# Kernel optimization log

Hardware: AMD Instinct MI355X
Metric: run time of the kernel (lower is better)

## Reference

```python
import jax, jax.numpy as jnp
import numpy as np

L = 32          # ss_num: number of sampled layers
D = 512         # lstm_size
OPS = 16        # operations_num
TEMP = 5.0
TANH_C = 2.5
OP_TANH_RED = 2.5
NEG = jnp.float32(-1e9)  # finite mask value (avoids inf/nan in grads)


def setup_inputs() -> dict:
    key = jax.random.key(0)
    ks = jax.random.split(key, 9)
    u = lambda k, s: jax.random.uniform(k, s, jnp.float32, -0.1, 0.1)  # reset_param: uniform(-0.1, 0.1)
    return {
        "embedding": u(ks[0], (OPS + 1, D)),
        "w_ih": u(ks[1], (4 * D, D)),
        "w_hh": u(ks[2], (4 * D, D)),
        "b_ih": u(ks[3], (4 * D,)),
        "b_hh": u(ks[4], (4 * D,)),
        "w_attn_1": u(ks[5], (D, D)),
        "w_attn_2": u(ks[6], (D, D)),
        "index_fc": u(ks[7], (D,)),
        "op_fc": u(ks[8], (OPS, D)),
    }


def _lstm_cell(x, h, c, w_ih, w_hh, b_ih, b_hh):
    # torch.nn.LSTMCell: gate order i, f, g, o
    g = x @ w_ih.T + b_ih + h @ w_hh.T + b_hh
    i, f, gg, o = jnp.split(g, 4, axis=-1)
    c2 = jax.nn.sigmoid(f) * c + jax.nn.sigmoid(i) * jnp.tanh(gg)
    h2 = jax.nn.sigmoid(o) * jnp.tanh(c2)
    return h2, c2


def reference(embedding, w_ih, w_hh, b_ih, b_hh, w_attn_1, w_attn_2, index_fc, op_fc):
    cell = lambda x, h, c: _lstm_cell(x, h, c, w_ih, w_hh, b_ih, b_hh)
    skey = jax.random.key(42)

    # --- initial construct_node (prev state = zeros) ---
    inp0 = embedding[OPS]                 # embedding of sentinel token [D]
    h, c = cell(inp0, jnp.zeros((D,), jnp.float32), jnp.zeros((D,), jnp.float32))
    anchors = jnp.zeros((L + 1, D), jnp.float32)            # anchor[0] = zeros_like(h)
    anchors_w1 = jnp.zeros((L + 1, D), jnp.float32).at[0].set(h @ w_attn_1.T)

    def step(carry, t):
        h, c, inp, anchors, anchors_w1, key = carry
        k1, k2, key = jax.random.split(key, 3)
        valid = jnp.arange(L + 1) <= t  # anchors 0..t exist at layer t

        # node selection
        h, c = cell(inp, h, c)
        query = jnp.tanh(anchors_w1 + h @ w_attn_2.T)        # [L+1, D]
        idx_logits = (query @ index_fc) / TEMP               # [L+1]
        idx_logits = TANH_C * jnp.tanh(idx_logits)
        idx_logits = jnp.where(valid, idx_logits, NEG)
        node_idx = jax.random.categorical(k1, idx_logits)
        lsm = jax.nn.log_softmax(idx_logits)
        node_lp = -lsm[node_idx]                             # cross_entropy
        node_ent = -jnp.sum(jnp.where(valid, lsm, 0.0) * jnp.exp(lsm))

        # op selection
        op_in = anchors[node_idx]
        h, c = cell(op_in, h, c)
        op_logits = (h @ op_fc.T) / TEMP
        op_logits = (TANH_C / OP_TANH_RED) * jnp.tanh(op_logits)
        op_idx = jax.random.categorical(k2, op_logits)
        olsm = jax.nn.log_softmax(op_logits)
        op_lp = -olsm[op_idx]
        op_ent = -jnp.sum(olsm * jnp.exp(olsm))

        inp = embedding[op_idx]
        anchors = anchors.at[t + 1].set(h)
        anchors_w1 = anchors_w1.at[t + 1].set(h @ w_attn_1.T)
        ent = jax.lax.stop_gradient(node_ent + op_ent)       # entropy is .detach()ed
        return (h, c, inp, anchors, anchors_w1, key), (node_idx, op_idx, node_lp + op_lp, ent)

    carry0 = (h, c, inp0, anchors, anchors_w1, skey)
    _, (nidx, oidx, lps, ents) = jax.lax.scan(step, carry0, jnp.arange(L))
    arch_seq = jnp.stack([nidx, oidx], axis=1).reshape(-1)   # interleave [node, op] x L
    return arch_seq, jnp.sum(ents), jnp.sum(lps)
```

## Files before the change

kernel.cpp:

```cpp
#include <hip/hip_runtime.h>
#include <stdint.h>


#define KWG    64
#define NTH    512
#define LSTEPS 32
#define DDIM   512
#define NOPS   16
#define NEGC   (-1.0e9f)

static __device__ __forceinline__ void tf2x32(uint32_t k0, uint32_t k1,
                                              uint32_t c0, uint32_t c1,
                                              uint32_t& o0, uint32_t& o1){
  uint32_t ks2 = k0 ^ k1 ^ 0x1BD11BDAu;
  uint32_t x0 = c0 + k0;
  uint32_t x1 = c1 + k1;
#define TFR(r) { x0 += x1; x1 = (x1 << (r)) | (x1 >> (32 - (r))); x1 ^= x0; }
  TFR(13) TFR(15) TFR(26) TFR(6)
  x0 += k1;  x1 += ks2 + 1u;
  TFR(17) TFR(29) TFR(16) TFR(24)
  x0 += ks2; x1 += k0 + 2u;
  TFR(13) TFR(15) TFR(26) TFR(6)
  x0 += k0;  x1 += k1 + 3u;
  TFR(17) TFR(29) TFR(16) TFR(24)
  x0 += k1;  x1 += ks2 + 4u;
  TFR(13) TFR(15) TFR(26) TFR(6)
  x0 += ks2; x1 += k0 + 5u;
#undef TFR
  o0 = x0; o1 = x1;
}

static __device__ __forceinline__ float gumbel_bits(uint32_t bits){
  float f = __uint_as_float((bits >> 9) | 0x3f800000u) - 1.0f;
  float u = (f == 0.0f) ? 1.1754943508222875e-38f : f;
  return -logf(-logf(u));
}

static __device__ __forceinline__ float sigm(float x){
  return 1.0f / (1.0f + expf(-x));
}

static __device__ __forceinline__ float wredsum(float v){
  #pragma unroll
  for (int m = 32; m; m >>= 1) v += __shfl_xor(v, m, 64);
  return v;
}

static __device__ __forceinline__ void gl8(const float* __restrict__ p, int lane, float* r){
  #pragma unroll
  for (int k = 0; k < 8; ++k) r[k] = p[(k << 6) + lane];
}

static __device__ __forceinline__ float dot8(const float* w, const float* x){
  float s = 0.f;
  #pragma unroll
  for (int k = 0; k < 8; ++k) s += w[k]*x[k];
  return s;
}

static __device__ __forceinline__ uint64_t tpack(uint32_t tag, float f){
  return ((uint64_t)tag << 32) | (uint64_t)__float_as_uint(f);
}
static __device__ __forceinline__ uint64_t ald64(const uint64_t* p){
  return __hip_atomic_load(p, __ATOMIC_RELAXED, __HIP_MEMORY_SCOPE_AGENT);
}
static __device__ __forceinline__ void ast64(uint64_t* p, uint64_t v){
  __hip_atomic_store(p, v, __ATOMIC_RELAXED, __HIP_MEMORY_SCOPE_AGENT);
}
static __device__ __forceinline__ float poll1(const uint64_t* p, uint32_t tag){
  uint64_t v = ald64(p);
  while ((uint32_t)(v >> 32) != tag){
    __builtin_amdgcn_s_sleep(1);
    v = ald64(p);
  }
  return __uint_as_float((uint32_t)v);
}
static __device__ __forceinline__ void poll8s(const uint64_t* base, int lane,
                                              uint32_t tag, float* r){
  uint64_t v[8];
  for (;;){
    #pragma unroll
    for (int k = 0; k < 8; ++k) v[k] = ald64(base + (k << 6) + lane);
    bool ok = true;
    #pragma unroll
    for (int k = 0; k < 8; ++k) ok &= ((uint32_t)(v[k] >> 32) == tag);
    if (ok) break;
    __builtin_amdgcn_s_sleep(1);
  }
  #pragma unroll
  for (int k = 0; k < 8; ++k) r[k] = __uint_as_float((uint32_t)v[k]);
}

__global__ void __launch_bounds__(NTH, 2)
Controller_60601988547087_kernel(const float* __restrict__ emb,
                                 const float* __restrict__ wih,
                                 const float* __restrict__ whh,
                                 const float* __restrict__ bih,
                                 const float* __restrict__ bhh,
                                 const float* __restrict__ wa1,
                                 const float* __restrict__ wa2,
                                 const float* __restrict__ idxfc,
                                 const float* __restrict__ opfc,
                                 float* __restrict__ out,
                                 uint64_t* __restrict__ ws64)
{
  const int tid  = threadIdx.x;
  const int wg   = blockIdx.x;
  const int wave = tid >> 6;
  const int lane = tid & 63;
  const int unit = (wg << 3) | wave;

  uint64_t* bufA64 = ws64;
  uint64_t* bufB64 = ws64 + 512;
  uint64_t* hw2g64 = ws64 + 1024;
  uint64_t* aw1g64 = ws64 + 1536;
  uint64_t* cand64 = ws64 + 1536 + 32*512;

  __shared__ float s_hc[DDIM];
  __shared__ float s_h1[DDIM];
  __shared__ float s_hw2[DDIM];
  __shared__ float s_xproj[17 * 32];
  __shared__ float s_aproj[33 * 33];
  __shared__ float s_opfc[NOPS * DDIM];
  __shared__ float s_logits[33];
  __shared__ float s_oplog[16];
  __shared__ int   s_ibc[2];

  float wihr[4][8], whhr[4][8], a1r[8], a2r[8], fcr[8], bsum[4];
  #pragma unroll
  for (int g = 0; g < 4; ++g){
    gl8(wih + (size_t)((g << 9) + unit) * DDIM, lane, wihr[g]);
    gl8(whh + (size_t)((g << 9) + unit) * DDIM, lane, whhr[g]);
    bsum[g] = bih[(g << 9) + unit] + bhh[(g << 9) + unit];
  }
  gl8(wa1 + (size_t)unit * DDIM, lane, a1r);
  gl8(wa2 + (size_t)unit * DDIM, lane, a2r);
  gl8(idxfc, lane, fcr);

  for (int i = tid; i < NOPS * DDIM; i += NTH) s_opfc[i] = opfc[i];
  if (tid < 33) s_aproj[tid] = 0.0f;

  for (int op = 0; op <= NOPS; ++op){
    float xc[8];
    gl8(emb + (size_t)op * DDIM, lane, xc);
    #pragma unroll
    for (int g = 0; g < 4; ++g){
      float xp = wredsum(dot8(wihr[g], xc));
      if (lane == 0) s_xproj[op * 32 + (wave << 2) + g] = xp;
    }
  }
  __syncthreads();

  float row0[8], row1[8], row2[8], row3[8];

  float cst;
  {
    const float* xp = s_xproj + 16 * 32 + (wave << 2);
    float gi = sigm(xp[0] + bsum[0]);
    float go = sigm(xp[3] + bsum[3]);
    cst = gi * tanhf(xp[2] + bsum[2]);
    float h0 = go * tanhf(cst);
    if (lane == 0) ast64(bufB64 + unit, tpack(1u, h0));
  }
  s_hc[tid] = poll1(bufB64 + tid, 1u);
  __syncthreads();

  uint32_t key0 = 0u, key1v = 42u;
  float ent_sum = 0.f, lp_sum = 0.f;
  int prev_op = NOPS;

  for (int t = 0; t < LSTEPS; ++t){
    const uint32_t tagA = 3u*(uint32_t)t + 2u;
    const uint32_t tagB = 3u*(uint32_t)t + 3u;
    const uint32_t tagK = 3u*(uint32_t)t + 4u;

    float hc8[8];
    gl8(s_hc, lane, hc8);

    {
      const float* xp = s_xproj + prev_op * 32 + (wave << 2);
      float p0 = wredsum(dot8(whhr[0], hc8));
      float p1 = wredsum(dot8(whhr[1], hc8));
      float p2 = wredsum(dot8(whhr[2], hc8));
      float p3 = wredsum(dot8(whhr[3], hc8));
      float gi = sigm(xp[0] + p0 + bsum[0]);
      float gf = sigm(xp[1] + p1 + bsum[1]);
      float go = sigm(xp[3] + p3 + bsum[3]);
      cst = gf * cst + gi * tanhf(xp[2] + p2 + bsum[2]);
      float hn = go * tanhf(cst);
      if (lane == 0) ast64(bufA64 + unit, tpack(tagA, hn));
    }
    {
      float pa = wredsum(dot8(a1r, hc8));
      if (lane == 0) ast64(aw1g64 + (size_t)t * DDIM + unit, tpack(tagA, pa));
      if (t > 0){
        #pragma unroll
        for (int g = 0; g < 4; ++g){
          float ap = wredsum(dot8(wihr[g], hc8));
          if (lane == 0) s_aproj[t * 33 + (wave << 2) + g] = ap;
        }
      }
    }
    if (wave == (t & 7)){
      const uint64_t* rb = aw1g64 + (size_t)t * DDIM;
      int slot = t >> 3;
      if      (slot == 0) poll8s(rb, lane, tagA, row0);
      else if (slot == 1) poll8s(rb, lane, tagA, row1);
      else if (slot == 2) poll8s(rb, lane, tagA, row2);
      else                poll8s(rb, lane, tagA, row3);
    }
    s_h1[tid] = poll1(bufA64 + tid, tagA);
    __syncthreads();

    float h18[8];
    gl8(s_h1, lane, h18);
    {
      float q = wredsum(dot8(a2r, h18));
      if (lane == 0) ast64(hw2g64 + unit, tpack(tagB, q));
    }
    float ghh0 = wredsum(dot8(whhr[0], h18));
    float ghh1 = wredsum(dot8(whhr[1], h18));
    float ghh2 = wredsum(dot8(whhr[2], h18));
    float ghh3 = wredsum(dot8(whhr[3], h18));
    float cst_cand = 0.f;
    if (lane <= t){
      const float* ag = s_aproj + lane * 33 + (wave << 2);
      float gi = sigm(ag[0] + ghh0 + bsum[0]);
      float gf = sigm(ag[1] + ghh1 + bsum[1]);
      float go = sigm(ag[3] + ghh3 + bsum[3]);
      cst_cand = gf * cst + gi * tanhf(ag[2] + ghh2 + bsum[2]);
      float h2c = go * tanhf(cst_cand);
      ast64(cand64 + (size_t)lane * DDIM + unit, tpack(tagK, h2c));
    }
    s_hw2[tid] = poll1(hw2g64 + tid, tagB);
    __syncthreads();

    int ni;
    float nlp_s = 0.f, nent_s = 0.f;
    uint32_t k2a_s = 0u, k2b_s = 0u;
    {
      float h2c[8];
      gl8(s_hw2, lane, h2c);
#define ROWDOT(RR, I)                                                          \
      { int i_ = (I);                                                          \
        if (i_ <= t){                                                          \
          float acc = 0.f;                                                     \
          _Pragma("unroll")                                                    \
          for (int k = 0; k < 8; ++k) acc += tanhf(RR[k] + h2c[k]) * fcr[k];   \
          acc = wredsum(acc);                                                  \
          if (lane == 0) s_logits[i_] = 2.5f * tanhf(acc / 5.0f);              \
        } }
      ROWDOT(row0, wave)
      ROWDOT(row1, wave + 8)
      ROWDOT(row2, wave + 16)
      ROWDOT(row3, wave + 24)
#undef ROWDOT
      __syncthreads();
      if (wave == 0){
        uint32_t s0 = 0, s1 = 0;
        if (lane < 3) tf2x32(key0, key1v, 0u, (uint32_t)lane, s0, s1);
        uint32_t k1a = __shfl(s0, 0, 64), k1b = __shfl(s1, 0, 64);
        k2a_s = __shfl(s0, 1, 64); k2b_s = __shfl(s1, 1, 64);
        uint32_t nk0 = __shfl(s0, 2, 64), nk1 = __shfl(s1, 2, 64);
        key0 = nk0; key1v = nk1;
        uint32_t y0 = 0, y1 = 0;
        if (lane < 33) tf2x32(k1a, k1b, 0u, (uint32_t)lane, y0, y1);
        uint32_t bits = y0 ^ y1;
        float gmb   = gumbel_bits(bits);
        float logit = (lane < 33) ? ((lane <= t) ? s_logits[lane] : NEGC) : -3.0e38f;
        float cand  = (lane < 33) ? (logit + gmb) : -3.0e38f;
        float v = cand; int bi = lane;
        #pragma unroll
        for (int m = 32; m; m >>= 1){
          float ov = __shfl_xor(v, m, 64); int ob = __shfl_xor(bi, m, 64);
          if (ov > v || (ov == v && ob < bi)){ v = ov; bi = ob; }
        }
        int ni_ = bi;
        float lm = (lane < 33) ? logit : -3.0e38f;
        #pragma unroll
        for (int m = 32; m; m >>= 1) lm = fmaxf(lm, __shfl_xor(lm, m, 64));
        float ex   = (lane < 33) ? expf(logit - lm) : 0.f;
        float ssum = wredsum(ex);
        float lsm  = logit - lm - logf(ssum);
        nlp_s  = -__shfl(lsm, ni_, 64);
        float entc = (lane <= t) ? (-lsm * expf(lsm)) : 0.f;
        nent_s = wredsum(entc);
        if (lane == 0) s_ibc[0] = ni_;
      }
      __syncthreads();
      ni = s_ibc[0];
    }

    cst = __shfl(cst_cand, ni, 64);
    s_hc[tid] = poll1(cand64 + (size_t)ni * DDIM + tid, tagK);
    __syncthreads();

    {
      float h28[8];
      gl8(s_hc, lane, h28);
      #pragma unroll
      for (int jj = 0; jj < 2; ++jj){
        int i = wave + (jj << 3);
        float acc = 0.f;
        #pragma unroll
        for (int k = 0; k < 8; ++k) acc += s_opfc[i * DDIM + (k << 6) + lane] * h28[k];
        acc = wredsum(acc);
        if (lane == 0) s_oplog[i] = tanhf(acc / 5.0f);
      }
      __syncthreads();
    }
    int oi;
    {
      if (wave == 0){
        uint32_t z0 = 0, z1 = 0;
        if (lane < 16) tf2x32(k2a_s, k2b_s, 0u, (uint32_t)lane, z0, z1);
        uint32_t bits = z0 ^ z1;
        float gmb   = gumbel_bits(bits);
        float logit = (lane < 16) ? s_oplog[lane] : -3.0e38f;
        float cand  = (lane < 16) ? (logit + gmb) : -3.0e38f;
        float v = cand; int bi = lane;
        #pragma unroll
        for (int m = 32; m; m >>= 1){
          float ov = __shfl_xor(v, m, 64); int ob = __shfl_xor(bi, m, 64);
          if (ov > v || (ov == v && ob < bi)){ v = ov; bi = ob; }
        }
        int oi_ = bi;
        float lm = (lane < 16) ? logit : -3.0e38f;
        #pragma unroll
        for (int m = 32; m; m >>= 1) lm = fmaxf(lm, __shfl_xor(lm, m, 64));
        float ex   = (lane < 16) ? expf(logit - lm) : 0.f;
        float ssum = wredsum(ex);
        float olsm = logit - lm - logf(ssum);
        float olp  = -__shfl(olsm, oi_, 64);
        float oent = wredsum((lane < 16) ? (-olsm * expf(olsm)) : 0.f);
        lp_sum  += nlp_s + olp;
        ent_sum += nent_s + oent;
        if (lane == 0){
          s_ibc[1] = oi_;
          if (wg == 0){
            out[2 * t]     = (float)ni;
            out[2 * t + 1] = (float)oi_;
          }
        }
      }
      __syncthreads();
      oi = s_ibc[1];
    }
    prev_op = oi;
  }

  if (wg == 0 && wave == 0 && lane == 0){
    out[64] = ent_sum;
    out[65] = lp_sum;
  }
}

extern "C" void kernel_launch(void* const* d_in, const int* in_sizes, int n_in,
                              void* d_out, int out_size, void* d_ws, size_t ws_size,
                              hipStream_t stream) {
  (void)in_sizes; (void)n_in; (void)out_size; (void)ws_size;
  const float* emb  = (const float*)d_in[0];
  const float* wih  = (const float*)d_in[1];
  const float* whh  = (const float*)d_in[2];
  const float* bih  = (const float*)d_in[3];
  const float* bhh  = (const float*)d_in[4];
  const float* wa1  = (const float*)d_in[5];
  const float* wa2  = (const float*)d_in[6];
  const float* ifc  = (const float*)d_in[7];
  const float* ofc  = (const float*)d_in[8];
  float* out = (float*)d_out;
  uint64_t* ws = (uint64_t*)d_ws;
  hipLaunchKernelGGL(Controller_60601988547087_kernel,
                     dim3(KWG), dim3(NTH), 0, stream,
                     emb, wih, whh, bih, bhh, wa1, wa2, ifc, ofc, out, ws);
}
```

Baseline: 417.5 us.

## Replace per-element tagged polling with per-workgroup flag barriers

The old scheme packed a tag with every float and had each thread spin on its own 64-bit element. The new scheme writes plain floats, drains stores, then sets one flag per workgroup and polls all 64 flags with a single wave before an acquire fence. Each wave then reads the shared vectors straight from global memory, with no LDS staging. This cuts the number of polled words and the LDS copy plus barrier per exchange. In exchange it adds a full grid-barrier style wait at each step and relies on the fence for correct ordering.

```diff
diff --git a/kernel.cpp b/kernel.cpp
--- a/kernel.cpp
+++ b/kernel.cpp
@@ -58,37 +58,23 @@
   return s;
 }
 
-static __device__ __forceinline__ uint64_t tpack(uint32_t tag, float f){
-  return ((uint64_t)tag << 32) | (uint64_t)__float_as_uint(f);
-}
-static __device__ __forceinline__ uint64_t ald64(const uint64_t* p){
+static __device__ __forceinline__ float agld(float* p){
   return __hip_atomic_load(p, __ATOMIC_RELAXED, __HIP_MEMORY_SCOPE_AGENT);
 }
-static __device__ __forceinline__ void ast64(uint64_t* p, uint64_t v){
+static __device__ __forceinline__ void agst(float* p, float v){
   __hip_atomic_store(p, v, __ATOMIC_RELAXED, __HIP_MEMORY_SCOPE_AGENT);
 }
-static __device__ __forceinline__ float poll1(const uint64_t* p, uint32_t tag){
-  uint64_t v = ald64(p);
-  while ((uint32_t)(v >> 32) != tag){
+static __device__ __forceinline__ void gld8(float* p, int lane, float* r){
+  #pragma unroll
+  for (int k = 0; k < 8; ++k) r[k] = agld(p + (k << 6) + lane);
+}
+static __device__ __forceinline__ void pollflag(uint32_t* f, int lane, uint32_t tag){
+  for (;;){
+    uint32_t v = __hip_atomic_load(f + lane, __ATOMIC_RELAXED, __HIP_MEMORY_SCOPE_AGENT);
+    if (__all(v == tag)) break;
     __builtin_amdgcn_s_sleep(1);
-    v = ald64(p);
-  }
-  return __uint_as_float((uint32_t)v);
-}
-static __device__ __forceinline__ void poll8s(const uint64_t* base, int lane,
-                                              uint32_t tag, float* r){
-  uint64_t v[8];
-  for (;;){
-    #pragma unroll
-    for (int k = 0; k < 8; ++k) v[k] = ald64(base + (k << 6) + lane);
-    bool ok = true;
-    #pragma unroll
-    for (int k = 0; k < 8; ++k) ok &= ((uint32_t)(v[k] >> 32) == tag);
-    if (ok) break;
-    __builtin_amdgcn_s_sleep(1);
-  }
-  #pragma unroll
-  for (int k = 0; k < 8; ++k) r[k] = __uint_as_float((uint32_t)v[k]);
+  }
+  __builtin_amdgcn_fence(__ATOMIC_ACQUIRE, "agent");
 }
 
 __global__ void __launch_bounds__(NTH, 2)
@@ -110,15 +96,14 @@
   const int lane = tid & 63;
   const int unit = (wg << 3) | wave;
 
-  uint64_t* bufA64 = ws64;
-  uint64_t* bufB64 = ws64 + 512;
-  uint64_t* hw2g64 = ws64 + 1024;
-  uint64_t* aw1g64 = ws64 + 1536;
-  uint64_t* cand64 = ws64 + 1536 + 32*512;
-
-  __shared__ float s_hc[DDIM];
-  __shared__ float s_h1[DDIM];
-  __shared__ float s_hw2[DDIM];
+  uint32_t* flagA = (uint32_t*)ws64;
+  uint32_t* flagB = flagA + 64;
+  float* h0f   = (float*)(ws64 + 64);
+  float* h1f   = h0f  + DDIM;
+  float* hw2f  = h1f  + DDIM;
+  float* aw1f  = hw2f + DDIM;
+  float* candf = aw1f + 32*DDIM;
+
   __shared__ float s_xproj[17 * 32];
   __shared__ float s_aproj[33 * 33];
   __shared__ float s_opfc[NOPS * DDIM];
@@ -160,22 +145,25 @@
     float go = sigm(xp[3] + bsum[3]);
     cst = gi * tanhf(xp[2] + bsum[2]);
     float h0 = go * tanhf(cst);
-    if (lane == 0) ast64(bufB64 + unit, tpack(1u, h0));
-  }
-  s_hc[tid] = poll1(bufB64 + tid, 1u);
+    if (lane == 0) agst(h0f + unit, h0);
+  }
+  asm volatile("s_waitcnt vmcnt(0)" ::: "memory");
   __syncthreads();
+  if (tid == 0)
+    __hip_atomic_store(flagA + wg, 1u, __ATOMIC_RELAXED, __HIP_MEMORY_SCOPE_AGENT);
+  if (wave == 0) pollflag(flagA, lane, 1u);
+  __syncthreads();
+
+  float hc8[8];
+  gld8(h0f, lane, hc8);
 
   uint32_t key0 = 0u, key1v = 42u;
   float ent_sum = 0.f, lp_sum = 0.f;
   int prev_op = NOPS;
 
   for (int t = 0; t < LSTEPS; ++t){
-    const uint32_t tagA = 3u*(uint32_t)t + 2u;
-    const uint32_t tagB = 3u*(uint32_t)t + 3u;
-    const uint32_t tagK = 3u*(uint32_t)t + 4u;
-
-    float hc8[8];
-    gl8(s_hc, lane, hc8);
+    const uint32_t tagA = 2u*(uint32_t)t + 2u;
+    const uint32_t tagB = 2u*(uint32_t)t + 3u;
 
     {
       const float* xp = s_xproj + prev_op * 32 + (wave << 2);
@@ -188,11 +176,9 @@
       float go = sigm(xp[3] + p3 + bsum[3]);
       cst = gf * cst + gi * tanhf(xp[2] + p2 + bsum[2]);
       float hn = go * tanhf(cst);
-      if (lane == 0) ast64(bufA64 + unit, tpack(tagA, hn));
-    }
-    {
+      if (lane == 0) agst(h1f + unit, hn);
       float pa = wredsum(dot8(a1r, hc8));
-      if (lane == 0) ast64(aw1g64 + (size_t)t * DDIM + unit, tpack(tagA, pa));
+      if (lane == 0) agst(aw1f + (size_t)t * DDIM + unit, pa);
       if (t > 0){
         #pragma unroll
         for (int g = 0; g < 4; ++g){
@@ -201,22 +187,27 @@
         }
       }
     }
+    asm volatile("s_waitcnt vmcnt(0)" ::: "memory");
+    __syncthreads();
+    if (tid == 0)
+      __hip_atomic_store(flagA + wg, tagA, __ATOMIC_RELAXED, __HIP_MEMORY_SCOPE_AGENT);
+    if (wave == 0) pollflag(flagA, lane, tagA);
+    __syncthreads();
+
     if (wave == (t & 7)){
-      const uint64_t* rb = aw1g64 + (size_t)t * DDIM;
+      float* rb = aw1f + (size_t)t * DDIM;
       int slot = t >> 3;
-      if      (slot == 0) poll8s(rb, lane, tagA, row0);
-      else if (slot == 1) poll8s(rb, lane, tagA, row1);
-      else if (slot == 2) poll8s(rb, lane, tagA, row2);
-      else                poll8s(rb, lane, tagA, row3);
-    }
-    s_h1[tid] = poll1(bufA64 + tid, tagA);
-    __syncthreads();
-
+      if      (slot == 0) gld8(rb, lane, row0);
+      else if (slot == 1) gld8(rb, lane, row1);
+      else if (slot == 2) gld8(rb, lane, row2);
+      else                gld8(rb, lane, row3);
+    }
     float h18[8];
-    gl8(s_h1, lane, h18);
+    gld8(h1f, lane, h18);
+
     {
       float q = wredsum(dot8(a2r, h18));
-      if (lane == 0) ast64(hw2g64 + unit, tpack(tagB, q));
+      if (lane == 0) agst(hw2f + unit, q);
     }
     float ghh0 = wredsum(dot8(whhr[0], h18));
     float ghh1 = wredsum(dot8(whhr[1], h18));
@@ -230,23 +221,27 @@
       float go = sigm(ag[3] + ghh3 + bsum[3]);
       cst_cand = gf * cst + gi * tanhf(ag[2] + ghh2 + bsum[2]);
       float h2c = go * tanhf(cst_cand);
-      ast64(cand64 + (size_t)lane * DDIM + unit, tpack(tagK, h2c));
-    }
-    s_hw2[tid] = poll1(hw2g64 + tid, tagB);
+      agst(candf + (size_t)lane * DDIM + unit, h2c);
+    }
+    asm volatile("s_waitcnt vmcnt(0)" ::: "memory");
+    __syncthreads();
+    if (tid == 0)
+      __hip_atomic_store(flagB + wg, tagB, __ATOMIC_RELAXED, __HIP_MEMORY_SCOPE_AGENT);
+    if (wave == 0) pollflag(flagB, lane, tagB);
     __syncthreads();
 
     int ni;
     float nlp_s = 0.f, nent_s = 0.f;
     uint32_t k2a_s = 0u, k2b_s = 0u;
     {
-      float h2c[8];
-      gl8(s_hw2, lane, h2c);
+      float hw28[8];
+      gld8(hw2f, lane, hw28);
 #define ROWDOT(RR, I)                                                          \
       { int i_ = (I);                                                          \
         if (i_ <= t){                                                          \
           float acc = 0.f;                                                     \
           _Pragma("unroll")                                                    \
-          for (int k = 0; k < 8; ++k) acc += tanhf(RR[k] + h2c[k]) * fcr[k];   \
+          for (int k = 0; k < 8; ++k) acc += tanhf(RR[k] + hw28[k]) * fcr[k];  \
           acc = wredsum(acc);                                                  \
           if (lane == 0) s_logits[i_] = 2.5f * tanhf(acc / 5.0f);              \
         } }
@@ -292,18 +287,15 @@
     }
 
     cst = __shfl(cst_cand, ni, 64);
-    s_hc[tid] = poll1(cand64 + (size_t)ni * DDIM + tid, tagK);
-    __syncthreads();
-
-    {
-      float h28[8];
-      gl8(s_hc, lane, h28);
+    gld8(candf + (size_t)ni * DDIM, lane, hc8);
+
+    {
       #pragma unroll
       for (int jj = 0; jj < 2; ++jj){
         int i = wave + (jj << 3);
         float acc = 0.f;
         #pragma unroll
-        for (int k = 0; k < 8; ++k) acc += s_opfc[i * DDIM + (k << 6) + lane] * h28[k];
+        for (int k = 0; k < 8; ++k) acc += s_opfc[i * DDIM + (k << 6) + lane] * hc8[k];
         acc = wredsum(acc);
         if (lane == 0) s_oplog[i] = tanhf(acc / 5.0f);
       }
```

Result: slower. 581.2 us (+39.2%).

## Replicate cross-workgroup exchange buffers per reader and spin without sleep

Applied to the files above, without the earlier changes.

Each producer wave now writes its value into 64 replicated slots, one per reader workgroup (8 replicas for candidate states), so each workgroup polls its own copy. The goal is to cut contention and coherence traffic from all workgroups polling the same global locations. The s_sleep calls in the polling loops are removed to lower wake-up latency. The aw1 buffer is no longer indexed by step, so it relies on tags to avoid overwrite races. Write traffic grows and busy spinning puts more pressure on the memory system.

```diff
diff --git a/kernel.cpp b/kernel.cpp
--- a/kernel.cpp
+++ b/kernel.cpp
@@ -69,10 +69,7 @@
 }
 static __device__ __forceinline__ float poll1(const uint64_t* p, uint32_t tag){
   uint64_t v = ald64(p);
-  while ((uint32_t)(v >> 32) != tag){
-    __builtin_amdgcn_s_sleep(1);
-    v = ald64(p);
-  }
+  while ((uint32_t)(v >> 32) != tag) v = ald64(p);
   return __uint_as_float((uint32_t)v);
 }
 static __device__ __forceinline__ void poll8s(const uint64_t* base, int lane,
@@ -85,7 +82,6 @@
     #pragma unroll
     for (int k = 0; k < 8; ++k) ok &= ((uint32_t)(v[k] >> 32) == tag);
     if (ok) break;
-    __builtin_amdgcn_s_sleep(1);
   }
   #pragma unroll
   for (int k = 0; k < 8; ++k) r[k] = __uint_as_float((uint32_t)v[k]);
@@ -110,11 +106,11 @@
   const int lane = tid & 63;
   const int unit = (wg << 3) | wave;
 
-  uint64_t* bufA64 = ws64;
-  uint64_t* bufB64 = ws64 + 512;
-  uint64_t* hw2g64 = ws64 + 1024;
-  uint64_t* aw1g64 = ws64 + 1536;
-  uint64_t* cand64 = ws64 + 1536 + 32*512;
+  uint64_t* h0_rep  = ws64;
+  uint64_t* h1_rep  = ws64 + 32768;
+  uint64_t* hw2_rep = ws64 + 2*32768;
+  uint64_t* aw1_rep = ws64 + 3*32768;
+  uint64_t* cand_rep= ws64 + 4*32768;
 
   __shared__ float s_hc[DDIM];
   __shared__ float s_h1[DDIM];
@@ -160,10 +156,12 @@
     float go = sigm(xp[3] + bsum[3]);
     cst = gi * tanhf(xp[2] + bsum[2]);
     float h0 = go * tanhf(cst);
-    if (lane == 0) ast64(bufB64 + unit, tpack(1u, h0));
-  }
-  s_hc[tid] = poll1(bufB64 + tid, 1u);
+    ast64(h0_rep + ((size_t)lane << 9) + unit, tpack(1u, h0));
+  }
+  s_hc[tid] = poll1(h0_rep + ((size_t)wg << 9) + tid, 1u);
   __syncthreads();
+  float hc8[8];
+  gl8(s_hc, lane, hc8);
 
   uint32_t key0 = 0u, key1v = 42u;
   float ent_sum = 0.f, lp_sum = 0.f;
@@ -173,9 +171,6 @@
     const uint32_t tagA = 3u*(uint32_t)t + 2u;
     const uint32_t tagB = 3u*(uint32_t)t + 3u;
     const uint32_t tagK = 3u*(uint32_t)t + 4u;
-
-    float hc8[8];
-    gl8(s_hc, lane, hc8);
 
     {
       const float* xp = s_xproj + prev_op * 32 + (wave << 2);
@@ -188,11 +183,9 @@
       float go = sigm(xp[3] + p3 + bsum[3]);
       cst = gf * cst + gi * tanhf(xp[2] + p2 + bsum[2]);
       float hn = go * tanhf(cst);
-      if (lane == 0) ast64(bufA64 + unit, tpack(tagA, hn));
-    }
-    {
+      ast64(h1_rep + ((size_t)lane << 9) + unit, tpack(tagA, hn));
       float pa = wredsum(dot8(a1r, hc8));
-      if (lane == 0) ast64(aw1g64 + (size_t)t * DDIM + unit, tpack(tagA, pa));
+      ast64(aw1_rep + ((size_t)lane << 9) + unit, tpack(tagA, pa));
       if (t > 0){
         #pragma unroll
         for (int g = 0; g < 4; ++g){
@@ -202,21 +195,21 @@
       }
     }
     if (wave == (t & 7)){
-      const uint64_t* rb = aw1g64 + (size_t)t * DDIM;
+      const uint64_t* rb = aw1_rep + ((size_t)wg << 9);
       int slot = t >> 3;
       if      (slot == 0) poll8s(rb, lane, tagA, row0);
       else if (slot == 1) poll8s(rb, lane, tagA, row1);
       else if (slot == 2) poll8s(rb, lane, tagA, row2);
       else                poll8s(rb, lane, tagA, row3);
     }
-    s_h1[tid] = poll1(bufA64 + tid, tagA);
+    s_h1[tid] = poll1(h1_rep + ((size_t)wg << 9) + tid, tagA);
     __syncthreads();
 
     float h18[8];
     gl8(s_h1, lane, h18);
     {
       float q = wredsum(dot8(a2r, h18));
-      if (lane == 0) ast64(hw2g64 + unit, tpack(tagB, q));
+      ast64(hw2_rep + ((size_t)lane << 9) + unit, tpack(tagB, q));
     }
     float ghh0 = wredsum(dot8(whhr[0], h18));
     float ghh1 = wredsum(dot8(whhr[1], h18));
@@ -230,9 +223,12 @@
       float go = sigm(ag[3] + ghh3 + bsum[3]);
       cst_cand = gf * cst + gi * tanhf(ag[2] + ghh2 + bsum[2]);
       float h2c = go * tanhf(cst_cand);
-      ast64(cand64 + (size_t)lane * DDIM + unit, tpack(tagK, h2c));
-    }
-    s_hw2[tid] = poll1(hw2g64 + tid, tagB);
+      #pragma unroll
+      for (int r = 0; r < 8; ++r)
+        ast64(cand_rep + (((size_t)r * 33 + (size_t)lane) << 9) + unit,
+              tpack(tagK, h2c));
+    }
+    s_hw2[tid] = poll1(hw2_rep + ((size_t)wg << 9) + tid, tagB);
     __syncthreads();
 
     int ni;
@@ -292,18 +288,18 @@
     }
 
     cst = __shfl(cst_cand, ni, 64);
-    s_hc[tid] = poll1(cand64 + (size_t)ni * DDIM + tid, tagK);
+    s_hc[tid] = poll1(cand_rep + (((size_t)(wg >> 3) * 33 + (size_t)ni) << 9) + tid,
+                      tagK);
     __syncthreads();
-
-    {
-      float h28[8];
-      gl8(s_hc, lane, h28);
+    gl8(s_hc, lane, hc8);
+
+    {
       #pragma unroll
       for (int jj = 0; jj < 2; ++jj){
         int i = wave + (jj << 3);
         float acc = 0.f;
         #pragma unroll
-        for (int k = 0; k < 8; ++k) acc += s_opfc[i * DDIM + (k << 6) + lane] * h28[k];
+        for (int k = 0; k < 8; ++k) acc += s_opfc[i * DDIM + (k << 6) + lane] * hc8[k];
         acc = wredsum(acc);
         if (lane == 0) s_oplog[i] = tanhf(acc / 5.0f);
       }
```

After: 596.3 us. 1.43x slower.
